# Kernel tuning notes

Hardware: AMD Instinct MI355X
Metric: run time of the kernel (lower is better)

Reference implementation:

```python
import jax, jax.numpy as jnp
import numpy as np

N, F_IN, F_OUT = 8192, 256, 256
EDGE_PROB = 0.004  # avg degree ~33


def setup_inputs() -> dict:
    key = jax.random.key(0)
    k1, k2, k3, k4 = jax.random.split(key, 4)
    X = jax.random.normal(k1, (N, F_IN), dtype=jnp.float32)
    # binary adjacency (any nonzero entry in the original is an edge)
    adj = (jax.random.uniform(k2, (N, N)) < EDGE_PROB).astype(jnp.float32)
    W = jax.random.normal(k3, (F_OUT, F_IN), dtype=jnp.float32) * 0.05
    b = jnp.zeros((F_OUT,), dtype=jnp.float32)
    S = jax.random.normal(k4, (2 * F_OUT,), dtype=jnp.float32) * 0.05
    return {"X": X, "adj": adj, "W": W, "b": b, "S": S}


def reference(X, adj, W, b, S):
    # X: [N, F_in], adj: [N, N], W: [F_out, F_in], b: [F_out], S: [2*F_out]
    Xp = X @ W.T + b                      # [N, F_out]
    f = Xp.shape[1]
    n = X.shape[0]
    # per-edge score e_ij = leaky_relu(Xp_i . S[:f] + Xp_j . S[f:])
    a_src = Xp @ S[:f]                    # [N]
    a_dst = Xp @ S[f:]                    # [N]
    e = jax.nn.leaky_relu(a_src[:, None] + a_dst[None, :])  # [N, N]
    # edges = nonzero(adj + I): self-loops always present
    mask = (adj != 0) | jnp.eye(n, dtype=bool)
    e = jnp.where(mask, e, -jnp.inf)
    # local (per-source-node) softmax over neighbors == segment softmax on i
    attn = jax.nn.softmax(e, axis=1)      # [N, N]
    return jax.nn.sigmoid(attn @ Xp)      # [N, F_out]
```

## Files before the change

### kernel.cpp

```cpp
#include <hip/hip_runtime.h>
#include <math.h>

#define NN 8192
#define FF 256
#define MAXN 128
#define NGEMM ((NN / 64) * (FF / 64))

__global__ __launch_bounds__(256) void gemm_scan_kernel(const float* __restrict__ X,
                                                        const float* __restrict__ W,
                                                        const float* __restrict__ bias,
                                                        const float* __restrict__ adj,
                                                        float* __restrict__ Xp,
                                                        int* __restrict__ cnt_g,
                                                        int* __restrict__ nbr_g) {
    __shared__ float Xs[64][64];
    __shared__ float Ws[64][64];
    __shared__ int   nbr_s[MAXN];
    __shared__ int   cnt;

    const int tid = threadIdx.x;

    if (blockIdx.x < NGEMM) {
        const int rt   = blockIdx.x >> 2;
        const int ct   = blockIdx.x & 3;
        const int row0 = rt * 64;
        const int col0 = ct * 64;
        const int ty   = tid >> 4;
        const int tx   = tid & 15;
        const int lrow = tid & 63;
        const int kq0  = (tid >> 6) * 4;

        const float* Xr = &X[(size_t)(row0 + lrow) * FF];
        const float* Wr = &W[(size_t)(col0 + lrow) * FF];

        float4 px[4], pw[4];
#pragma unroll
        for (int q = 0; q < 4; ++q) {
            px[q] = *reinterpret_cast<const float4*>(&Xr[(kq0 + q) * 4]);
            pw[q] = *reinterpret_cast<const float4*>(&Wr[(kq0 + q) * 4]);
        }

        float acc[4][4] = {};

#pragma unroll
        for (int kt = 0; kt < 4; ++kt) {
#pragma unroll
            for (int q = 0; q < 4; ++q) {
                const int k0 = (kq0 + q) * 4;
                Xs[k0+0][lrow]=px[q].x; Xs[k0+1][lrow]=px[q].y; Xs[k0+2][lrow]=px[q].z; Xs[k0+3][lrow]=px[q].w;
                Ws[k0+0][lrow]=pw[q].x; Ws[k0+1][lrow]=pw[q].y; Ws[k0+2][lrow]=pw[q].z; Ws[k0+3][lrow]=pw[q].w;
            }
            __syncthreads();
            if (kt < 3) {
                const int kb = (kt + 1) * 64;
#pragma unroll
                for (int q = 0; q < 4; ++q) {
                    px[q] = *reinterpret_cast<const float4*>(&Xr[kb + (kq0 + q) * 4]);
                    pw[q] = *reinterpret_cast<const float4*>(&Wr[kb + (kq0 + q) * 4]);
                }
            }
#pragma unroll 8
            for (int k = 0; k < 64; ++k) {
                const float4 a4 = *reinterpret_cast<const float4*>(&Xs[k][ty * 4]);
                const float4 b4 = *reinterpret_cast<const float4*>(&Ws[k][tx * 4]);
                const float av[4] = {a4.x, a4.y, a4.z, a4.w};
                const float bv[4] = {b4.x, b4.y, b4.z, b4.w};
#pragma unroll
                for (int ii = 0; ii < 4; ++ii)
#pragma unroll
                    for (int jj = 0; jj < 4; ++jj)
                        acc[ii][jj] = fmaf(av[ii], bv[jj], acc[ii][jj]);
            }
            __syncthreads();
        }

        const float4 b4 = *reinterpret_cast<const float4*>(&bias[col0 + tx * 4]);
#pragma unroll
        for (int ii = 0; ii < 4; ++ii) {
            const int r = row0 + ty * 4 + ii;
            float4 o;
            o.x = acc[ii][0] + b4.x;
            o.y = acc[ii][1] + b4.y;
            o.z = acc[ii][2] + b4.z;
            o.w = acc[ii][3] + b4.w;
            *reinterpret_cast<float4*>(&Xp[(size_t)r * FF + col0 + tx * 4]) = o;
        }
    } else {
        const int i = blockIdx.x - NGEMM;
        if (tid == 0) cnt = 0;
        __syncthreads();

        const size_t base = (size_t)i * NN;
        float4 v[8];
#pragma unroll
        for (int it = 0; it < 8; ++it)
            v[it] = *reinterpret_cast<const float4*>(&adj[base + it * 1024 + tid * 4]);
#pragma unroll
        for (int it = 0; it < 8; ++it) {
            const int c0 = it * 1024 + tid * 4;
            const float vv[4] = {v[it].x, v[it].y, v[it].z, v[it].w};
#pragma unroll
            for (int u = 0; u < 4; ++u) {
                const int col = c0 + u;
                if (vv[u] != 0.f || col == i) {
                    const int slot = atomicAdd(&cnt, 1);
                    if (slot < MAXN) nbr_s[slot] = col;
                }
            }
        }
        __syncthreads();
        const int n = min(cnt, MAXN);
        if (tid < n) nbr_g[(size_t)i * MAXN + tid] = nbr_s[tid];
        if (tid == 0) cnt_g[i] = n;
    }
}

__global__ __launch_bounds__(256) void dots_kernel(const float* __restrict__ Xp,
                                                   const float* __restrict__ S,
                                                   float* __restrict__ a_src,
                                                   float* __restrict__ a_dst) {
    const int wid  = threadIdx.x >> 6;
    const int lane = threadIdx.x & 63;
    const int row  = blockIdx.x * 4 + wid;
    const float4 xv = *reinterpret_cast<const float4*>(&Xp[(size_t)row * FF + lane * 4]);
    const float4 s0 = *reinterpret_cast<const float4*>(&S[lane * 4]);
    const float4 s1 = *reinterpret_cast<const float4*>(&S[FF + lane * 4]);
    float ps = xv.x * s0.x + xv.y * s0.y + xv.z * s0.z + xv.w * s0.w;
    float pd = xv.x * s1.x + xv.y * s1.y + xv.z * s1.z + xv.w * s1.w;
#pragma unroll
    for (int off = 32; off; off >>= 1) {
        ps += __shfl_xor(ps, off);
        pd += __shfl_xor(pd, off);
    }
    if (lane == 0) {
        a_src[row] = ps;
        a_dst[row] = pd;
    }
}

__global__ __launch_bounds__(256) void agg_kernel(const int* __restrict__ cnt_g,
                                                  const int* __restrict__ nbr_g,
                                                  const float* __restrict__ a_src,
                                                  const float* __restrict__ a_dst,
                                                  const float* __restrict__ Xp,
                                                  float* __restrict__ out) {
    __shared__ int   nb[4][MAXN];
    __shared__ float wt[4][MAXN];

    const int wid  = threadIdx.x >> 6;
    const int lane = threadIdx.x & 63;
    const int i    = blockIdx.x * 4 + wid;

    const int   n  = cnt_g[i];
    const float si = a_src[i];

    int   j0 = 0, j1 = 0;
    float e0 = -INFINITY, e1 = -INFINITY;
    if (lane < n) {
        j0 = nbr_g[(size_t)i * MAXN + lane];
        const float x = si + a_dst[j0];
        e0 = (x >= 0.f) ? x : 0.01f * x;
    }
    if (lane + 64 < n) {
        j1 = nbr_g[(size_t)i * MAXN + lane + 64];
        const float x = si + a_dst[j1];
        e1 = (x >= 0.f) ? x : 0.01f * x;
    }

    float m = fmaxf(e0, e1);
#pragma unroll
    for (int off = 32; off; off >>= 1) m = fmaxf(m, __shfl_xor(m, off));

    const float w0 = (lane < n)      ? __expf(e0 - m) : 0.f;
    const float w1 = (lane + 64 < n) ? __expf(e1 - m) : 0.f;
    float s = w0 + w1;
#pragma unroll
    for (int off = 32; off; off >>= 1) s += __shfl_xor(s, off);
    const float inv_den = 1.f / s;

    nb[wid][lane]      = j0;
    wt[wid][lane]      = w0 * inv_den;
    nb[wid][lane + 64] = j1;
    wt[wid][lane + 64] = w1 * inv_den;
    __syncthreads();

    const float* xb = Xp + lane * 4;
    float4 acc = {0.f, 0.f, 0.f, 0.f};
    int k = 0;
    for (; k + 2 <= n; k += 2) {
        const int   g0 = nb[wid][k],     g1 = nb[wid][k + 1];
        const float u0 = wt[wid][k],     u1 = wt[wid][k + 1];
        const float4 v0 = *reinterpret_cast<const float4*>(&xb[(size_t)g0 * FF]);
        const float4 v1 = *reinterpret_cast<const float4*>(&xb[(size_t)g1 * FF]);
        acc.x += u0 * v0.x + u1 * v1.x;
        acc.y += u0 * v0.y + u1 * v1.y;
        acc.z += u0 * v0.z + u1 * v1.z;
        acc.w += u0 * v0.w + u1 * v1.w;
    }
    if (k < n) {
        const int   g0 = nb[wid][k];
        const float u0 = wt[wid][k];
        const float4 v0 = *reinterpret_cast<const float4*>(&xb[(size_t)g0 * FF]);
        acc.x += u0 * v0.x; acc.y += u0 * v0.y; acc.z += u0 * v0.z; acc.w += u0 * v0.w;
    }

    float4 o;
    o.x = 1.f / (1.f + __expf(-acc.x));
    o.y = 1.f / (1.f + __expf(-acc.y));
    o.z = 1.f / (1.f + __expf(-acc.z));
    o.w = 1.f / (1.f + __expf(-acc.w));
    *reinterpret_cast<float4*>(&out[(size_t)i * FF + lane * 4]) = o;
}

extern "C" void kernel_launch(void* const* d_in, const int* in_sizes, int n_in,
                              void* d_out, int out_size, void* d_ws, size_t ws_size,
                              hipStream_t stream) {
    const float* X   = (const float*)d_in[0];
    const float* adj = (const float*)d_in[1];
    const float* W   = (const float*)d_in[2];
    const float* b   = (const float*)d_in[3];
    const float* S   = (const float*)d_in[4];
    float* out = (float*)d_out;

    float* Xp    = (float*)d_ws;
    float* a_src = Xp + (size_t)NN * FF;
    float* a_dst = a_src + NN;
    int*   cnt_g = (int*)(a_dst + NN);
    int*   nbr_g = cnt_g + NN;

    gemm_scan_kernel<<<NGEMM + NN, 256, 0, stream>>>(X, W, b, adj, Xp, cnt_g, nbr_g);
    dots_kernel<<<NN / 4, 256, 0, stream>>>(Xp, S, a_src, a_dst);
    agg_kernel<<<NN / 4, 256, 0, stream>>>(cnt_g, nbr_g, a_src, a_dst, Xp, out);
}
```

Baseline: 398.4 us.

## Split adjacency scan in halves and overlap second half with aggregation

The adjacency row scan is split into two halves. The first half still runs alongside the GEMM. The second half now runs in the same launch as aggregation of the first half's rows, and a final kernel aggregates the remaining rows. The goal is to overlap the bandwidth-heavy adj streaming with the gather-bound aggregation, instead of putting all of the scan before the dependent kernels. Removing __syncthreads from the aggregation path depends on each wave touching only its own shared slice. The change also adds a fourth kernel launch.

```diff
diff --git a/kernel.cpp b/kernel.cpp
--- a/kernel.cpp
+++ b/kernel.cpp
@@ -4,20 +4,115 @@
 #define NN 8192
 #define FF 256
 #define MAXN 128
+#define HALF (NN / 2)
 #define NGEMM ((NN / 64) * (FF / 64))
 
-__global__ __launch_bounds__(256) void gemm_scan_kernel(const float* __restrict__ X,
-                                                        const float* __restrict__ W,
-                                                        const float* __restrict__ bias,
-                                                        const float* __restrict__ adj,
-                                                        float* __restrict__ Xp,
-                                                        int* __restrict__ cnt_g,
-                                                        int* __restrict__ nbr_g) {
+__device__ __forceinline__ void scan_row(const float* __restrict__ adj, int i, int tid,
+                                         int* nbr_s, int* cnt_s,
+                                         int* __restrict__ cnt_g, int* __restrict__ nbr_g) {
+    if (tid == 0) *cnt_s = 0;
+    __syncthreads();
+    const size_t base = (size_t)i * NN;
+    float4 v[8];
+#pragma unroll
+    for (int it = 0; it < 8; ++it)
+        v[it] = *reinterpret_cast<const float4*>(&adj[base + it * 1024 + tid * 4]);
+#pragma unroll
+    for (int it = 0; it < 8; ++it) {
+        const int c0 = it * 1024 + tid * 4;
+        const float vv[4] = {v[it].x, v[it].y, v[it].z, v[it].w};
+#pragma unroll
+        for (int u = 0; u < 4; ++u) {
+            const int col = c0 + u;
+            if (vv[u] != 0.f || col == i) {
+                const int slot = atomicAdd(cnt_s, 1);
+                if (slot < MAXN) nbr_s[slot] = col;
+            }
+        }
+    }
+    __syncthreads();
+    const int n = min(*cnt_s, MAXN);
+    if (tid < n) nbr_g[(size_t)i * MAXN + tid] = nbr_s[tid];
+    if (tid == 0) cnt_g[i] = n;
+}
+
+__device__ __forceinline__ void agg_row(int i, int lane,
+                                        int* nb, float* wt,
+                                        const int* __restrict__ cnt_g,
+                                        const int* __restrict__ nbr_g,
+                                        const float* __restrict__ a_src,
+                                        const float* __restrict__ a_dst,
+                                        const float* __restrict__ Xp,
+                                        float* __restrict__ out) {
+    const int   n  = cnt_g[i];
+    const float si = a_src[i];
+
+    int   j0 = 0, j1 = 0;
+    float e0 = -INFINITY, e1 = -INFINITY;
+    if (lane < n) {
+        j0 = nbr_g[(size_t)i * MAXN + lane];
+        const float x = si + a_dst[j0];
+        e0 = (x >= 0.f) ? x : 0.01f * x;
+    }
+    if (lane + 64 < n) {
+        j1 = nbr_g[(size_t)i * MAXN + lane + 64];
+        const float x = si + a_dst[j1];
+        e1 = (x >= 0.f) ? x : 0.01f * x;
+    }
+
+    float m = fmaxf(e0, e1);
+#pragma unroll
+    for (int off = 32; off; off >>= 1) m = fmaxf(m, __shfl_xor(m, off));
+
+    const float w0 = (lane < n)      ? __expf(e0 - m) : 0.f;
+    const float w1 = (lane + 64 < n) ? __expf(e1 - m) : 0.f;
+    float s = w0 + w1;
+#pragma unroll
+    for (int off = 32; off; off >>= 1) s += __shfl_xor(s, off);
+    const float inv_den = 1.f / s;
+
+    nb[lane]      = j0;
+    wt[lane]      = w0 * inv_den;
+    nb[lane + 64] = j1;
+    wt[lane + 64] = w1 * inv_den;
+
+    const float* xb = Xp + lane * 4;
+    float4 acc = {0.f, 0.f, 0.f, 0.f};
+    int k = 0;
+    for (; k + 2 <= n; k += 2) {
+        const int   g0 = nb[k],     g1 = nb[k + 1];
+        const float u0 = wt[k],     u1 = wt[k + 1];
+        const float4 v0 = *reinterpret_cast<const float4*>(&xb[(size_t)g0 * FF]);
+        const float4 v1 = *reinterpret_cast<const float4*>(&xb[(size_t)g1 * FF]);
+        acc.x += u0 * v0.x + u1 * v1.x;
+        acc.y += u0 * v0.y + u1 * v1.y;
+        acc.z += u0 * v0.z + u1 * v1.z;
+        acc.w += u0 * v0.w + u1 * v1.w;
+    }
+    if (k < n) {
+        const int   g0 = nb[k];
+        const float u0 = wt[k];
+        const float4 v0 = *reinterpret_cast<const float4*>(&xb[(size_t)g0 * FF]);
+        acc.x += u0 * v0.x; acc.y += u0 * v0.y; acc.z += u0 * v0.z; acc.w += u0 * v0.w;
+    }
+
+    float4 o;
+    o.x = 1.f / (1.f + __expf(-acc.x));
+    o.y = 1.f / (1.f + __expf(-acc.y));
+    o.z = 1.f / (1.f + __expf(-acc.z));
+    o.w = 1.f / (1.f + __expf(-acc.w));
+    *reinterpret_cast<float4*>(&out[(size_t)i * FF + lane * 4]) = o;
+}
+
+__global__ __launch_bounds__(256) void gemm_scanA_kernel(const float* __restrict__ X,
+                                                         const float* __restrict__ W,
+                                                         const float* __restrict__ bias,
+                                                         const float* __restrict__ adj,
+                                                         float* __restrict__ Xp,
+                                                         int* __restrict__ cnt_g,
+                                                         int* __restrict__ nbr_g) {
     __shared__ float Xs[64][64];
     __shared__ float Ws[64][64];
-    __shared__ int   nbr_s[MAXN];
-    __shared__ int   cnt;
-
     const int tid = threadIdx.x;
 
     if (blockIdx.x < NGEMM) {
@@ -86,32 +181,9 @@
             *reinterpret_cast<float4*>(&Xp[(size_t)r * FF + col0 + tx * 4]) = o;
         }
     } else {
-        const int i = blockIdx.x - NGEMM;
-        if (tid == 0) cnt = 0;
-        __syncthreads();
-
-        const size_t base = (size_t)i * NN;
-        float4 v[8];
-#pragma unroll
-        for (int it = 0; it < 8; ++it)
-            v[it] = *reinterpret_cast<const float4*>(&adj[base + it * 1024 + tid * 4]);
-#pragma unroll
-        for (int it = 0; it < 8; ++it) {
-            const int c0 = it * 1024 + tid * 4;
-            const float vv[4] = {v[it].x, v[it].y, v[it].z, v[it].w};
-#pragma unroll
-            for (int u = 0; u < 4; ++u) {
-                const int col = c0 + u;
-                if (vv[u] != 0.f || col == i) {
-                    const int slot = atomicAdd(&cnt, 1);
-                    if (slot < MAXN) nbr_s[slot] = col;
-                }
-            }
-        }
-        __syncthreads();
-        const int n = min(cnt, MAXN);
-        if (tid < n) nbr_g[(size_t)i * MAXN + tid] = nbr_s[tid];
-        if (tid == 0) cnt_g[i] = n;
+        __shared__ int nbr_s[MAXN];
+        __shared__ int cnt;
+        scan_row(adj, blockIdx.x - NGEMM, tid, nbr_s, &cnt, cnt_g, nbr_g);
     }
 }
 
@@ -138,78 +210,42 @@
     }
 }
 
-__global__ __launch_bounds__(256) void agg_kernel(const int* __restrict__ cnt_g,
-                                                  const int* __restrict__ nbr_g,
-                                                  const float* __restrict__ a_src,
-                                                  const float* __restrict__ a_dst,
-                                                  const float* __restrict__ Xp,
-                                                  float* __restrict__ out) {
+__global__ __launch_bounds__(256) void aggA_scanB_kernel(const float* __restrict__ adj,
+                                                         const int* __restrict__ cnt_g,
+                                                         const int* __restrict__ nbr_g,
+                                                         const float* __restrict__ a_src,
+                                                         const float* __restrict__ a_dst,
+                                                         const float* __restrict__ Xp,
+                                                         float* __restrict__ out,
+                                                         int* __restrict__ cnt_gw,
+                                                         int* __restrict__ nbr_gw) {
+    const int tid = threadIdx.x;
+    if (blockIdx.x < HALF / 4) {
+        __shared__ int   nb[4][MAXN];
+        __shared__ float wt[4][MAXN];
+        const int wid  = tid >> 6;
+        const int lane = tid & 63;
+        const int i    = blockIdx.x * 4 + wid;
+        agg_row(i, lane, nb[wid], wt[wid], cnt_g, nbr_g, a_src, a_dst, Xp, out);
+    } else {
+        __shared__ int nbr_s[MAXN];
+        __shared__ int cnt;
+        scan_row(adj, HALF + (blockIdx.x - HALF / 4), tid, nbr_s, &cnt, cnt_gw, nbr_gw);
+    }
+}
+
+__global__ __launch_bounds__(256) void aggB_kernel(const int* __restrict__ cnt_g,
+                                                   const int* __restrict__ nbr_g,
+                                                   const float* __restrict__ a_src,
+                                                   const float* __restrict__ a_dst,
+                                                   const float* __restrict__ Xp,
+                                                   float* __restrict__ out) {
     __shared__ int   nb[4][MAXN];
     __shared__ float wt[4][MAXN];
-
     const int wid  = threadIdx.x >> 6;
     const int lane = threadIdx.x & 63;
-    const int i    = blockIdx.x * 4 + wid;
-
-    const int   n  = cnt_g[i];
-    const float si = a_src[i];
-
-    int   j0 = 0, j1 = 0;
-    float e0 = -INFINITY, e1 = -INFINITY;
-    if (lane < n) {
-        j0 = nbr_g[(size_t)i * MAXN + lane];
-        const float x = si + a_dst[j0];
-        e0 = (x >= 0.f) ? x : 0.01f * x;
-    }
-    if (lane + 64 < n) {
-        j1 = nbr_g[(size_t)i * MAXN + lane + 64];
-        const float x = si + a_dst[j1];
-        e1 = (x >= 0.f) ? x : 0.01f * x;
-    }
-
-    float m = fmaxf(e0, e1);
-#pragma unroll
-    for (int off = 32; off; off >>= 1) m = fmaxf(m, __shfl_xor(m, off));
-
-    const float w0 = (lane < n)      ? __expf(e0 - m) : 0.f;
-    const float w1 = (lane + 64 < n) ? __expf(e1 - m) : 0.f;
-    float s = w0 + w1;
-#pragma unroll
-    for (int off = 32; off; off >>= 1) s += __shfl_xor(s, off);
-    const float inv_den = 1.f / s;
-
-    nb[wid][lane]      = j0;
-    wt[wid][lane]      = w0 * inv_den;
-    nb[wid][lane + 64] = j1;
-    wt[wid][lane + 64] = w1 * inv_den;
-    __syncthreads();
-
-    const float* xb = Xp + lane * 4;
-    float4 acc = {0.f, 0.f, 0.f, 0.f};
-    int k = 0;
-    for (; k + 2 <= n; k += 2) {
-        const int   g0 = nb[wid][k],     g1 = nb[wid][k + 1];
-        const float u0 = wt[wid][k],     u1 = wt[wid][k + 1];
-        const float4 v0 = *reinterpret_cast<const float4*>(&xb[(size_t)g0 * FF]);
-        const float4 v1 = *reinterpret_cast<const float4*>(&xb[(size_t)g1 * FF]);
-        acc.x += u0 * v0.x + u1 * v1.x;
-        acc.y += u0 * v0.y + u1 * v1.y;
-        acc.z += u0 * v0.z + u1 * v1.z;
-        acc.w += u0 * v0.w + u1 * v1.w;
-    }
-    if (k < n) {
-        const int   g0 = nb[wid][k];
-        const float u0 = wt[wid][k];
-        const float4 v0 = *reinterpret_cast<const float4*>(&xb[(size_t)g0 * FF]);
-        acc.x += u0 * v0.x; acc.y += u0 * v0.y; acc.z += u0 * v0.z; acc.w += u0 * v0.w;
-    }
-
-    float4 o;
-    o.x = 1.f / (1.f + __expf(-acc.x));
-    o.y = 1.f / (1.f + __expf(-acc.y));
-    o.z = 1.f / (1.f + __expf(-acc.z));
-    o.w = 1.f / (1.f + __expf(-acc.w));
-    *reinterpret_cast<float4*>(&out[(size_t)i * FF + lane * 4]) = o;
+    const int i    = HALF + blockIdx.x * 4 + wid;
+    agg_row(i, lane, nb[wid], wt[wid], cnt_g, nbr_g, a_src, a_dst, Xp, out);
 }
 
 extern "C" void kernel_launch(void* const* d_in, const int* in_sizes, int n_in,
@@ -228,7 +264,9 @@
     int*   cnt_g = (int*)(a_dst + NN);
     int*   nbr_g = cnt_g + NN;
 
-    gemm_scan_kernel<<<NGEMM + NN, 256, 0, stream>>>(X, W, b, adj, Xp, cnt_g, nbr_g);
+    gemm_scanA_kernel<<<NGEMM + HALF, 256, 0, stream>>>(X, W, b, adj, Xp, cnt_g, nbr_g);
     dots_kernel<<<NN / 4, 256, 0, stream>>>(Xp, S, a_src, a_dst);
-    agg_kernel<<<NN / 4, 256, 0, stream>>>(cnt_g, nbr_g, a_src, a_dst, Xp, out);
-}
+    aggA_scanB_kernel<<<HALF / 4 + HALF, 256, 0, stream>>>(adj, cnt_g, nbr_g, a_src, a_dst,
+                                                           Xp, out, cnt_g, nbr_g);
+    aggB_kernel<<<HALF / 4, 256, 0, stream>>>(cnt_g, nbr_g, a_src, a_dst, Xp, out);
+}
```

Measured after the change: 399.0 us. Within noise of the previous version (+0.1%).

## Fuse attention-score dots into GEMM epilogue and interleave GEMM with scan blocks

Applied to the files above, without the earlier changes.

Removes the separate dots kernel. Each GEMM tile now computes partial a_src/a_dst dot products in its epilogue and accumulates them with atomics into arrays zeroed by a memset. Block indices are interleaved so every 17th block is a GEMM tile and the rest scan adjacency rows, spreading compute-bound and bandwidth-bound work across the GPU. It also drops a __syncthreads in the aggregation kernel, which is safe because each wavefront reads only its own shared-memory slice. The costs are an extra memset launch, atomics, and nondeterministic summation order for the scores.

```diff
diff --git a/kernel.cpp b/kernel.cpp
--- a/kernel.cpp
+++ b/kernel.cpp
@@ -6,23 +6,25 @@
 #define MAXN 128
 #define NGEMM ((NN / 64) * (FF / 64))
 
-__global__ __launch_bounds__(256) void gemm_scan_kernel(const float* __restrict__ X,
-                                                        const float* __restrict__ W,
-                                                        const float* __restrict__ bias,
-                                                        const float* __restrict__ adj,
-                                                        float* __restrict__ Xp,
-                                                        int* __restrict__ cnt_g,
-                                                        int* __restrict__ nbr_g) {
+__global__ __launch_bounds__(256) void gemm_scan_dots_kernel(const float* __restrict__ X,
+                                                             const float* __restrict__ W,
+                                                             const float* __restrict__ bias,
+                                                             const float* __restrict__ S,
+                                                             const float* __restrict__ adj,
+                                                             float* __restrict__ Xp,
+                                                             float* __restrict__ a_src,
+                                                             float* __restrict__ a_dst,
+                                                             int* __restrict__ cnt_g,
+                                                             int* __restrict__ nbr_g) {
     __shared__ float Xs[64][64];
     __shared__ float Ws[64][64];
-    __shared__ int   nbr_s[MAXN];
-    __shared__ int   cnt;
-
     const int tid = threadIdx.x;
-
-    if (blockIdx.x < NGEMM) {
-        const int rt   = blockIdx.x >> 2;
-        const int ct   = blockIdx.x & 3;
+    const int bid = blockIdx.x;
+    const int q17 = bid / 17;
+
+    if (bid % 17 == 0) {
+        const int rt   = q17 >> 2;
+        const int ct   = q17 & 3;
         const int row0 = rt * 64;
         const int col0 = ct * 64;
         const int ty   = tid >> 4;
@@ -74,7 +76,9 @@
             __syncthreads();
         }
 
-        const float4 b4 = *reinterpret_cast<const float4*>(&bias[col0 + tx * 4]);
+        const float4 b4  = *reinterpret_cast<const float4*>(&bias[col0 + tx * 4]);
+        const float4 s0v = *reinterpret_cast<const float4*>(&S[col0 + tx * 4]);
+        const float4 s1v = *reinterpret_cast<const float4*>(&S[FF + col0 + tx * 4]);
 #pragma unroll
         for (int ii = 0; ii < 4; ++ii) {
             const int r = row0 + ty * 4 + ii;
@@ -84,9 +88,23 @@
             o.z = acc[ii][2] + b4.z;
             o.w = acc[ii][3] + b4.w;
             *reinterpret_cast<float4*>(&Xp[(size_t)r * FF + col0 + tx * 4]) = o;
+
+            float ps = o.x * s0v.x + o.y * s0v.y + o.z * s0v.z + o.w * s0v.w;
+            float pd = o.x * s1v.x + o.y * s1v.y + o.z * s1v.z + o.w * s1v.w;
+#pragma unroll
+            for (int off = 8; off; off >>= 1) {
+                ps += __shfl_xor(ps, off);
+                pd += __shfl_xor(pd, off);
+            }
+            if (tx == 0) {
+                atomicAdd(&a_src[r], ps);
+                atomicAdd(&a_dst[r], pd);
+            }
         }
     } else {
-        const int i = blockIdx.x - NGEMM;
+        __shared__ int nbr_s[MAXN];
+        __shared__ int cnt;
+        const int i = bid - q17 - 1;
         if (tid == 0) cnt = 0;
         __syncthreads();
 
@@ -112,29 +130,6 @@
         const int n = min(cnt, MAXN);
         if (tid < n) nbr_g[(size_t)i * MAXN + tid] = nbr_s[tid];
         if (tid == 0) cnt_g[i] = n;
-    }
-}
-
-__global__ __launch_bounds__(256) void dots_kernel(const float* __restrict__ Xp,
-                                                   const float* __restrict__ S,
-                                                   float* __restrict__ a_src,
-                                                   float* __restrict__ a_dst) {
-    const int wid  = threadIdx.x >> 6;
-    const int lane = threadIdx.x & 63;
-    const int row  = blockIdx.x * 4 + wid;
-    const float4 xv = *reinterpret_cast<const float4*>(&Xp[(size_t)row * FF + lane * 4]);
-    const float4 s0 = *reinterpret_cast<const float4*>(&S[lane * 4]);
-    const float4 s1 = *reinterpret_cast<const float4*>(&S[FF + lane * 4]);
-    float ps = xv.x * s0.x + xv.y * s0.y + xv.z * s0.z + xv.w * s0.w;
-    float pd = xv.x * s1.x + xv.y * s1.y + xv.z * s1.z + xv.w * s1.w;
-#pragma unroll
-    for (int off = 32; off; off >>= 1) {
-        ps += __shfl_xor(ps, off);
-        pd += __shfl_xor(pd, off);
-    }
-    if (lane == 0) {
-        a_src[row] = ps;
-        a_dst[row] = pd;
     }
 }
 
@@ -182,14 +177,13 @@
     wt[wid][lane]      = w0 * inv_den;
     nb[wid][lane + 64] = j1;
     wt[wid][lane + 64] = w1 * inv_den;
-    __syncthreads();
 
     const float* xb = Xp + lane * 4;
     float4 acc = {0.f, 0.f, 0.f, 0.f};
     int k = 0;
     for (; k + 2 <= n; k += 2) {
-        const int   g0 = nb[wid][k],     g1 = nb[wid][k + 1];
-        const float u0 = wt[wid][k],     u1 = wt[wid][k + 1];
+        const int   g0 = nb[wid][k],  g1 = nb[wid][k + 1];
+        const float u0 = wt[wid][k],  u1 = wt[wid][k + 1];
         const float4 v0 = *reinterpret_cast<const float4*>(&xb[(size_t)g0 * FF]);
         const float4 v1 = *reinterpret_cast<const float4*>(&xb[(size_t)g1 * FF]);
         acc.x += u0 * v0.x + u1 * v1.x;
@@ -228,7 +222,8 @@
     int*   cnt_g = (int*)(a_dst + NN);
     int*   nbr_g = cnt_g + NN;
 
-    gemm_scan_kernel<<<NGEMM + NN, 256, 0, stream>>>(X, W, b, adj, Xp, cnt_g, nbr_g);
-    dots_kernel<<<NN / 4, 256, 0, stream>>>(Xp, S, a_src, a_dst);
+    hipMemsetAsync(a_src, 0, 2 * NN * sizeof(float), stream);
+    gemm_scan_dots_kernel<<<NGEMM + NN, 256, 0, stream>>>(X, W, b, S, adj, Xp,
+                                                          a_src, a_dst, cnt_g, nbr_g);
     agg_kernel<<<NN / 4, 256, 0, stream>>>(cnt_g, nbr_g, a_src, a_dst, Xp, out);
 }
```

After: 410.2 us. 1.03x slower.
